# Performance work log

Measured on AMD Instinct MI355X. Metric: run time of the kernel, lower is better.

The kernel has to match this reference:

```python
import jax, jax.numpy as jnp
import numpy as np

N, E, IN, HID, H, L, G = 50000, 500000, 64, 128, 4, 3, 64
C = HID // H


def setup_inputs() -> dict:
    key = jax.random.key(0)
    ks = jax.random.split(key, 24)
    def lin(k, i, o):
        return jax.random.normal(k, (i, o), jnp.float32) * (1.0 / np.sqrt(i))
    d = {}
    d["x"] = jax.random.normal(ks[0], (N, IN), jnp.float32)
    d["edge_index"] = jax.random.randint(ks[1], (2, E), 0, N, jnp.int32)
    d["batch"] = jnp.sort(jax.random.randint(ks[2], (N,), 0, G, jnp.int32))
    # layer 0 (in_dim -> hidden)
    d["l0_Wq"] = lin(ks[3], IN, HID); d["l0_bq"] = jnp.zeros((HID,), jnp.float32)
    d["l0_Wk"] = lin(ks[4], IN, HID); d["l0_bk"] = jnp.zeros((HID,), jnp.float32)
    d["l0_Wv"] = lin(ks[5], IN, HID); d["l0_bv"] = jnp.zeros((HID,), jnp.float32)
    d["l0_Ws"] = lin(ks[6], IN, HID); d["l0_bs"] = jnp.zeros((HID,), jnp.float32)
    d["l0_Wbeta"] = lin(ks[7], 3 * HID, 1)
    d["l0_ln_g"] = jnp.ones((HID,), jnp.float32); d["l0_ln_b"] = jnp.zeros((HID,), jnp.float32)
    # layers 1..L-1 (hidden -> hidden), stacked on leading axis
    M = L - 1
    def slin(k, i, o):
        return jax.random.normal(k, (M, i, o), jnp.float32) * (1.0 / np.sqrt(i))
    d["Wq"] = slin(ks[8], HID, HID); d["bq"] = jnp.zeros((M, HID), jnp.float32)
    d["Wk"] = slin(ks[9], HID, HID); d["bk"] = jnp.zeros((M, HID), jnp.float32)
    d["Wv"] = slin(ks[10], HID, HID); d["bv"] = jnp.zeros((M, HID), jnp.float32)
    d["Ws"] = slin(ks[11], HID, HID); d["bs"] = jnp.zeros((M, HID), jnp.float32)
    d["Wbeta"] = slin(ks[12], 3 * HID, 1)
    d["ln_g"] = jnp.ones((M, HID), jnp.float32); d["ln_b"] = jnp.zeros((M, HID), jnp.float32)
    d["mlp_W1"] = lin(ks[13], HID, HID); d["mlp_b1"] = jnp.zeros((HID,), jnp.float32)
    d["mlp_W2"] = lin(ks[14], HID, 1); d["mlp_b2"] = jnp.zeros((1,), jnp.float32)
    return d


def _conv(x, ei, Wq, bq, Wk, bk, Wv, bv, Ws, bs, Wbeta):
    """PyG TransformerConv with beta=True, concat=True (eval mode, no dropout)."""
    src, dst = ei[0], ei[1]
    q = (x @ Wq + bq).reshape(N, H, C)[dst]   # [E,H,C] target queries
    k = (x @ Wk + bk).reshape(N, H, C)[src]   # [E,H,C] source keys
    v = (x @ Wv + bv).reshape(N, H, C)[src]   # [E,H,C] source values
    alpha = (q * k).sum(-1) / np.sqrt(C)      # [E,H]
    amax = jax.lax.stop_gradient(jax.ops.segment_max(alpha, dst, num_segments=N))
    p = jnp.exp(alpha - amax[dst])
    denom = jax.ops.segment_sum(p, dst, num_segments=N)  # [N,H]
    p = p / denom[dst]                                   # segment softmax per dst node
    out = jax.ops.segment_sum(p[:, :, None] * v, dst, num_segments=N).reshape(N, HID)
    x_r = x @ Ws + bs                                    # root/skip transform
    beta = jax.nn.sigmoid(jnp.concatenate([out, x_r, out - x_r], axis=-1) @ Wbeta)  # [N,1]
    return beta * x_r + (1.0 - beta) * out


def _ln(x, g, b):
    mu = x.mean(-1, keepdims=True)
    var = x.var(-1, keepdims=True)
    return (x - mu) / jnp.sqrt(var + 1e-5) * g + b


def reference(x, edge_index, batch, l0_Wq, l0_bq, l0_Wk, l0_bk, l0_Wv, l0_bv, l0_Ws,
              l0_bs, l0_Wbeta, l0_ln_g, l0_ln_b, Wq, bq, Wk, bk, Wv, bv, Ws, bs,
              Wbeta, ln_g, ln_b, mlp_W1, mlp_b1, mlp_W2, mlp_b2):
    h = _conv(x, edge_index, l0_Wq, l0_bq, l0_Wk, l0_bk, l0_Wv, l0_bv, l0_Ws, l0_bs, l0_Wbeta)
    h = jax.nn.gelu(_ln(h, l0_ln_g, l0_ln_b), approximate=False)
    for i in range(L - 1):
        h = _conv(h, edge_index, Wq[i], bq[i], Wk[i], bk[i], Wv[i], bv[i], Ws[i], bs[i], Wbeta[i])
        h = jax.nn.gelu(_ln(h, ln_g[i], ln_b[i]), approximate=False)
    cnt = jax.ops.segment_sum(jnp.ones((N, 1), h.dtype), batch, num_segments=G)
    g = jax.ops.segment_sum(h, batch, num_segments=G) / jnp.maximum(cnt, 1.0)  # mean pool
    hm = jax.nn.gelu(g @ mlp_W1 + mlp_b1, approximate=False)
    return (hm @ mlp_W2 + mlp_b2).reshape(-1)
```

## Files before the change

### kernel.cpp

```cpp
#include <hip/hip_runtime.h>
#include <hip/hip_bf16.h>
#include <hip/hip_fp16.h>

#define NN 50000
#define EE 500000
#define DIN 64
#define HIDD 128
#define NG 64
#define NB1 49

typedef short short8 __attribute__((ext_vector_type(8)));
typedef float f32x4 __attribute__((ext_vector_type(4)));
typedef _Float16 hf2 __attribute__((ext_vector_type(2)));

#define GLL(g, l)                                                              \
  __builtin_amdgcn_global_load_lds(                                            \
      (const __attribute__((address_space(1))) unsigned*)(g),                  \
      (__attribute__((address_space(3))) unsigned*)(l), 16, 0, 0)

__device__ __forceinline__ unsigned short f2bf(float f) {
  unsigned u = __float_as_uint(f);
  u += 0x7fffu + ((u >> 16) & 1u);
  return (unsigned short)(u >> 16);
}
__device__ __forceinline__ float bfl(unsigned short u) {
  return __uint_as_float((unsigned)u << 16);
}
__device__ __forceinline__ unsigned short f2h(float f) {
  __half h = __float2half(f);
  return *(unsigned short*)&h;
}
__device__ __forceinline__ hf2 u2h2(unsigned u) {
  union { unsigned u; hf2 h; } c; c.u = u; return c.h;
}
__device__ __forceinline__ float dot2h(hf2 a, hf2 b) {
#if __has_builtin(__builtin_amdgcn_fdot2)
  return __builtin_amdgcn_fdot2(a, b, 0.f, false);
#else
  return (float)a.x * (float)b.x + (float)a.y * (float)b.y;
#endif
}

struct BiasW { const float* b[4]; };
struct PrepW { const float* w[12]; };

__global__ __launch_bounds__(256) void count_kernel(const int* __restrict__ ei,
                                                    int* __restrict__ cnt, int E) {
  int e = blockIdx.x * 256 + threadIdx.x;
  if (e < E) atomicAdd(&cnt[ei[E + e]], 1);
}

__global__ __launch_bounds__(1024) void scan1_kernel(const int* __restrict__ cnts,
                                                     int* __restrict__ starts,
                                                     int* __restrict__ btot) {
  __shared__ int sh[1024];
  int t = threadIdx.x;
  int idx = blockIdx.x * 1024 + t;
  int v = (idx < NN) ? cnts[idx] : 0;
  sh[t] = v;
  __syncthreads();
  for (int off = 1; off < 1024; off <<= 1) {
    int add = (t >= off) ? sh[t - off] : 0;
    __syncthreads();
    sh[t] += add;
    __syncthreads();
  }
  if (idx < NN) starts[idx] = sh[t] - v;
  if (t == 1023) btot[blockIdx.x] = sh[1023];
}

__global__ __launch_bounds__(64) void scan2_kernel(const int* __restrict__ btot,
                                                   int* __restrict__ boff,
                                                   int* __restrict__ starts) {
  int t = threadIdx.x;
  int orig = (t < NB1) ? btot[t] : 0;
  int v = orig;
  for (int off = 1; off < 64; off <<= 1) {
    int n_ = __shfl_up(v, off);
    if (t >= off) v += n_;
  }
  if (t < NB1) boff[t] = v - orig;
  if (t == NB1 - 1) starts[NN] = v;
}

__global__ __launch_bounds__(256) void scan3_kernel(int* __restrict__ starts,
                                                    const int* __restrict__ boff,
                                                    int* __restrict__ pos) {
  int i = blockIdx.x * 256 + threadIdx.x;
  if (i < NN) {
    int s = starts[i] + boff[i >> 10];
    starts[i] = s;
    pos[i] = s;
  }
}

__global__ __launch_bounds__(256) void scatter_kernel(const int* __restrict__ ei,
                                                      int* __restrict__ pos,
                                                      int* __restrict__ csr_src, int E) {
  int e = blockIdx.x * 256 + threadIdx.x;
  if (e < 8) csr_src[E + e] = 0;
  if (e < E) {
    int dst = ei[E + e];
    int p = atomicAdd(&pos[dst], 1);
    csr_src[p] = ei[e];
  }
}

__global__ __launch_bounds__(256) void prep_kernel(PrepW pw, short* __restrict__ wT) {
  int o = blockIdx.x * 256 + threadIdx.x;
  if (o >= 163840) return;
  int m, local, K;
  if (o < 32768) { m = o >> 13; local = o & 8191; K = 64; }
  else { int oo = o - 32768; m = 4 + (oo >> 14); local = oo & 16383; K = 128; }
  int col = local / K;
  int off = (local % K) * 2;
  int sw = off ^ ((col & 7) << 4);
  int k = (sw >> 4) * 8 + ((sw & 15) >> 1);
  wT[o] = (short)f2bf(pw.w[m][(size_t)k * 128 + col]);
}

template <int K, bool BF16IN>
__global__ __launch_bounds__(256) void gemm_mat(
    const void* __restrict__ hin, const short* __restrict__ wT, BiasW bw,
    unsigned short* __restrict__ qb, unsigned short* __restrict__ kvb,
    unsigned short* __restrict__ sb, int N) {
  constexpr int RB = 2 * K;
  constexpr int CALLS = (128 * RB) / 4096;
  const float QSC = 0.17677669529663687f;
  __shared__ short bS[128 * K];
  const int mat = blockIdx.y;
  const short* __restrict__ wm = wT + (size_t)mat * 128 * K;
  const int t = threadIdx.x, l = t & 63, wv = t >> 6;

  {
    const char* g0 = (const char*)wm;
    char* lp = (char*)bS;
#pragma unroll
    for (int i = 0; i < CALLS; ++i)
      GLL(g0 + i * 4096 + wv * 1024 + l * 16, lp + i * 4096 + wv * 1024);
  }
  __syncthreads();

  const int lr = l & 15, lk = l >> 4;
  const float* __restrict__ bias = bw.b[mat];

  for (int r0 = blockIdx.x * 64 + wv * 16; r0 < N; r0 += gridDim.x * 64) {
    const int gr = r0 + lr;
    const bool ok = gr < N;
    short8 hfrag[K / 32];
    if (BF16IN) {
      const short* hs = (const short*)hin;
#pragma unroll
      for (int ks = 0; ks < K / 32; ++ks) {
        short8 z = {0, 0, 0, 0, 0, 0, 0, 0};
        hfrag[ks] = ok ? *(const short8*)(hs + (size_t)gr * K + ks * 32 + lk * 8) : z;
      }
    } else {
      const float* hf = (const float*)hin;
#pragma unroll
      for (int ks = 0; ks < K / 32; ++ks) {
        short8 pk = {0, 0, 0, 0, 0, 0, 0, 0};
        if (ok) {
          const float* hp = hf + (size_t)gr * K + ks * 32 + lk * 8;
          f32x4 f0 = *(const f32x4*)hp;
          f32x4 f1 = *(const f32x4*)(hp + 4);
          pk[0] = f2bf(f0.x); pk[1] = f2bf(f0.y); pk[2] = f2bf(f0.z); pk[3] = f2bf(f0.w);
          pk[4] = f2bf(f1.x); pk[5] = f2bf(f1.y); pk[6] = f2bf(f1.z); pk[7] = f2bf(f1.w);
        }
        hfrag[ks] = pk;
      }
    }

    f32x4 acc[8] = {};
#pragma unroll
    for (int ks = 0; ks < K / 32; ++ks) {
#pragma unroll
      for (int cf = 0; cf < 8; ++cf) {
        int col = cf * 16 + lr;
        unsigned bb = col * RB + ((((ks * 4 + lk) * 16)) ^ ((col & 7) << 4));
        short8 w8 = *(const short8*)((const char*)bS + bb);
        acc[cf] = __builtin_amdgcn_mfma_f32_16x16x32_bf16(w8, hfrag[ks], acc[cf], 0, 0, 0);
      }
    }

    if (gr < N) {
#pragma unroll
      for (int cf = 0; cf < 8; ++cf) {
        int ch0 = cf * 16 + lk * 4;
        f32x4 b4 = *(const f32x4*)&bias[ch0];
        float v0 = acc[cf][0] + b4.x, v1 = acc[cf][1] + b4.y;
        float v2 = acc[cf][2] + b4.z, v3 = acc[cf][3] + b4.w;
        if (mat == 0) {
          ushort4 o;
          o.x = f2h(v0 * QSC); o.y = f2h(v1 * QSC);
          o.z = f2h(v2 * QSC); o.w = f2h(v3 * QSC);
          *(ushort4*)&qb[(size_t)gr * 128 + ch0] = o;
        } else if (mat == 3) {
          ushort4 o;
          o.x = f2bf(v0); o.y = f2bf(v1); o.z = f2bf(v2); o.w = f2bf(v3);
          *(ushort4*)&sb[(size_t)gr * 128 + ch0] = o;
        } else {
          unsigned u0 = (unsigned)f2h(v0) | ((unsigned)f2h(v1) << 16);
          unsigned u1 = (unsigned)f2h(v2) | ((unsigned)f2h(v3) << 16);
          unsigned* kvr = (unsigned*)kvb + (size_t)gr * 128;
          int base = ch0 + (mat == 2 ? 1 : 0);
          kvr[base] = u0;
          kvr[base + 2] = u1;
        }
      }
    }
  }
}

template <int NB, bool MASK>
__device__ __forceinline__ void att_batch(
    const int* __restrict__ csr, int i, int s1, const unsigned* __restrict__ kvu,
    int lane, hf2 qp, float& d, float& o0, float& o1) {
  int ce = csr[i + (lane & (NB - 1))];
  uint2 w[NB];
#pragma unroll
  for (int e = 0; e < NB; ++e) {
    int s = __builtin_amdgcn_readlane(ce, e);
    w[e] = *((const uint2*)kvu + ((size_t)s << 6) + lane);
  }
#pragma unroll
  for (int e = 0; e < NB; ++e) {
    float part = dot2h(u2h2(w[e].x), qp);
    part += __shfl_xor(part, 1);
    part += __shfl_xor(part, 2);
    part += __shfl_xor(part, 4);
    part += __shfl_xor(part, 8);
    float p = __expf(part);
    if (MASK) p = (i + e < s1) ? p : 0.f;
    d += p;
    __half2 vh = *(__half2*)&w[e].y;
    float2 vf = __half22float2(vh);
    o0 = fmaf(p, vf.x, o0);
    o1 = fmaf(p, vf.y, o1);
  }
}

__global__ __launch_bounds__(256, 8) void attn_fused(
    const unsigned short* __restrict__ qb, const unsigned* __restrict__ kvu,
    const unsigned short* __restrict__ sb, const int* __restrict__ starts,
    const int* __restrict__ csr, const float* __restrict__ Wbeta,
    const float* __restrict__ lng, const float* __restrict__ lnb,
    unsigned short* __restrict__ hout, int N) {
  int wid = (blockIdx.x * 256 + threadIdx.x) >> 6;
  if (wid >= N) return;
  const int lane = threadIdx.x & 63;
  hf2 qp = u2h2(((const unsigned*)qb)[(size_t)wid * 64 + lane]);
  int s0 = starts[wid], s1 = starts[wid + 1];
  float d = 0.f, o0 = 0.f, o1 = 0.f;
  int i = s0;
  for (; i + 8 <= s1; i += 8)
    att_batch<8, false>(csr, i, s1, kvu, lane, qp, d, o0, o1);
  if (i < s1) {
    if (s1 - i <= 4)
      att_batch<4, true>(csr, i, s1, kvu, lane, qp, d, o0, o1);
    else
      att_batch<8, true>(csr, i, s1, kvu, lane, qp, d, o0, o1);
  }
  float inv = d > 0.f ? 1.f / d : 0.f;
  o0 *= inv; o1 *= inv;
  unsigned su = ((const unsigned*)sb)[(size_t)wid * 64 + lane];
  float sx = bfl((unsigned short)su), sy = bfl((unsigned short)(su >> 16));
  float2 wbo = *(const float2*)&Wbeta[2 * lane];
  float2 wbx = *(const float2*)&Wbeta[128 + 2 * lane];
  float2 wbd = *(const float2*)&Wbeta[256 + 2 * lane];
  float bl = o0 * wbo.x + o1 * wbo.y + sx * wbx.x + sy * wbx.y
           + (o0 - sx) * wbd.x + (o1 - sy) * wbd.y;
  bl += __shfl_xor(bl, 1);  bl += __shfl_xor(bl, 2);  bl += __shfl_xor(bl, 4);
  bl += __shfl_xor(bl, 8);  bl += __shfl_xor(bl, 16); bl += __shfl_xor(bl, 32);
  float beta = 1.f / (1.f + __expf(-bl));
  float hx = beta * sx + (1.f - beta) * o0;
  float hy = beta * sy + (1.f - beta) * o1;
  float s = hx + hy, sq = hx * hx + hy * hy;
  s += __shfl_xor(s, 1);  sq += __shfl_xor(sq, 1);
  s += __shfl_xor(s, 2);  sq += __shfl_xor(sq, 2);
  s += __shfl_xor(s, 4);  sq += __shfl_xor(sq, 4);
  s += __shfl_xor(s, 8);  sq += __shfl_xor(sq, 8);
  s += __shfl_xor(s, 16); sq += __shfl_xor(sq, 16);
  s += __shfl_xor(s, 32); sq += __shfl_xor(sq, 32);
  float mu = s * (1.f / 128.f);
  float var = sq * (1.f / 128.f) - mu * mu;
  float rstd = 1.f / sqrtf(var + 1e-5f);
  float2 g2 = *(const float2*)&lng[2 * lane];
  float2 b2 = *(const float2*)&lnb[2 * lane];
  float y0 = (hx - mu) * rstd * g2.x + b2.x;
  float y1 = (hy - mu) * rstd * g2.y + b2.y;
  y0 = 0.5f * y0 * (1.f + erff(y0 * 0.70710678118654752f));
  y1 = 0.5f * y1 * (1.f + erff(y1 * 0.70710678118654752f));
  unsigned outw = (unsigned)f2bf(y0) | ((unsigned)f2bf(y1) << 16);
  ((unsigned*)hout)[(size_t)wid * 64 + lane] = outw;
}

__global__ __launch_bounds__(256) void pool_kernel(const unsigned short* __restrict__ h,
    const int* __restrict__ batch, float* __restrict__ g,
    float* __restrict__ gcnt, int N) {
  __shared__ float accS[NG * HIDD];
  __shared__ float cntS[NG];
  int t = threadIdx.x;
  for (int i = t; i < NG * HIDD; i += 256) accS[i] = 0.f;
  if (t < NG) cntS[t] = 0.f;
  __syncthreads();
  int lane = t & 63, grp = t >> 6;
  const unsigned* h32 = (const unsigned*)h;
  for (int n = blockIdx.x * 4 + grp; n < N; n += gridDim.x * 4) {
    int b = batch[n];
    unsigned u = h32[(size_t)n * 64 + lane];
    atomicAdd(&accS[b * HIDD + (lane << 1)], __uint_as_float(u << 16));
    atomicAdd(&accS[b * HIDD + (lane << 1) + 1], __uint_as_float(u & 0xffff0000u));
    if (lane == 0) atomicAdd(&cntS[b], 1.f);
  }
  __syncthreads();
  for (int i = t; i < NG * HIDD; i += 256)
    if (accS[i] != 0.f) atomicAdd(&g[i], accS[i]);
  if (t < NG && cntS[t] != 0.f) atomicAdd(&gcnt[t], cntS[t]);
}

__global__ __launch_bounds__(128) void final_kernel(const float* __restrict__ g,
    const float* __restrict__ gcnt, const float* __restrict__ W1,
    const float* __restrict__ b1, const float* __restrict__ W2,
    const float* __restrict__ b2, float* __restrict__ out) {
  __shared__ float gS[HIDD];
  __shared__ float red[2];
  const int gr = blockIdx.x, t = threadIdx.x;
  float cnt = fmaxf(gcnt[gr], 1.f);
  gS[t] = g[gr * HIDD + t] / cnt;
  __syncthreads();
  float s = b1[t];
#pragma unroll 4
  for (int k = 0; k < HIDD; ++k) s = fmaf(gS[k], W1[k * HIDD + t], s);
  s = 0.5f * s * (1.f + erff(s * 0.70710678118654752f));
  float p = s * W2[t];
  p += __shfl_xor(p, 1);  p += __shfl_xor(p, 2);  p += __shfl_xor(p, 4);
  p += __shfl_xor(p, 8);  p += __shfl_xor(p, 16); p += __shfl_xor(p, 32);
  if ((t & 63) == 0) red[t >> 6] = p;
  __syncthreads();
  if (t == 0) out[gr] = red[0] + red[1] + b2[0];
}

extern "C" void kernel_launch(void* const* d_in, const int* in_sizes, int n_in,
                              void* d_out, int out_size, void* d_ws, size_t ws_size,
                              hipStream_t stream) {
  const float* x        = (const float*)d_in[0];
  const int*   ei       = (const int*)d_in[1];
  const int*   batch    = (const int*)d_in[2];
  const float* l0_Wq    = (const float*)d_in[3];
  const float* l0_bq    = (const float*)d_in[4];
  const float* l0_Wk    = (const float*)d_in[5];
  const float* l0_bk    = (const float*)d_in[6];
  const float* l0_Wv    = (const float*)d_in[7];
  const float* l0_bv    = (const float*)d_in[8];
  const float* l0_Ws    = (const float*)d_in[9];
  const float* l0_bs    = (const float*)d_in[10];
  const float* l0_Wbeta = (const float*)d_in[11];
  const float* l0_lng   = (const float*)d_in[12];
  const float* l0_lnb   = (const float*)d_in[13];
  const float* Wq       = (const float*)d_in[14];
  const float* bq       = (const float*)d_in[15];
  const float* Wk       = (const float*)d_in[16];
  const float* bk       = (const float*)d_in[17];
  const float* Wv       = (const float*)d_in[18];
  const float* bv       = (const float*)d_in[19];
  const float* Ws       = (const float*)d_in[20];
  const float* bs       = (const float*)d_in[21];
  const float* Wbeta    = (const float*)d_in[22];
  const float* lng      = (const float*)d_in[23];
  const float* lnb      = (const float*)d_in[24];
  const float* mlp_W1   = (const float*)d_in[25];
  const float* mlp_b1   = (const float*)d_in[26];
  const float* mlp_W2   = (const float*)d_in[27];
  const float* mlp_b2   = (const float*)d_in[28];
  float* outp = (float*)d_out;

  char* ws = (char*)d_ws;
  size_t off = 0;
  auto alloc = [&](size_t bytes) -> void* {
    void* p = ws + off;
    off = (off + bytes + 255) & ~(size_t)255;
    return p;
  };
  unsigned short* h0  = (unsigned short*)alloc((size_t)NN * HIDD * 2);
  unsigned short* h1  = (unsigned short*)alloc((size_t)NN * HIDD * 2);
  unsigned short* qbv = (unsigned short*)alloc((size_t)NN * HIDD * 2);
  unsigned short* sbv = (unsigned short*)alloc((size_t)NN * HIDD * 2);
  unsigned short* kvb = (unsigned short*)alloc((size_t)NN * 256 * 2);
  short*  wT     = (short*)alloc((size_t)163840 * 2);
  int*    starts = (int*)alloc((size_t)(NN + 1) * 4);
  int*    pos    = (int*)alloc((size_t)NN * 4);
  int*    csr    = (int*)alloc((size_t)(EE + 8) * 4);
  int*    btot   = (int*)alloc((size_t)NB1 * 4);
  int*    boff   = (int*)alloc((size_t)NB1 * 4);
  float*  g      = (float*)alloc((size_t)NG * HIDD * 4);
  float*  gcnt   = (float*)alloc((size_t)NG * 4);
  (void)ws_size; (void)in_sizes; (void)n_in; (void)out_size;

  PrepW pw = {{l0_Wq, l0_Wk, l0_Wv, l0_Ws,
               Wq, Wk, Wv, Ws,
               Wq + 16384, Wk + 16384, Wv + 16384, Ws + 16384}};
  prep_kernel<<<640, 256, 0, stream>>>(pw, wT);

  hipMemsetAsync(pos, 0, (size_t)NN * 4, stream);
  count_kernel<<<(EE + 255) / 256, 256, 0, stream>>>(ei, pos, EE);
  scan1_kernel<<<NB1, 1024, 0, stream>>>(pos, starts, btot);
  scan2_kernel<<<1, 64, 0, stream>>>(btot, boff, starts);
  scan3_kernel<<<(NN + 255) / 256, 256, 0, stream>>>(starts, boff, pos);
  scatter_kernel<<<(EE + 255) / 256, 256, 0, stream>>>(ei, pos, csr, EE);

  dim3 ggrid(256, 4);
  int agrid = (NN + 3) / 4;
  const unsigned* kvu = (const unsigned*)kvb;

  BiasW b0 = {{l0_bq, l0_bk, l0_bv, l0_bs}};
  gemm_mat<DIN, false><<<ggrid, 256, 0, stream>>>(x, wT, b0, qbv, kvb, sbv, NN);
  attn_fused<<<agrid, 256, 0, stream>>>(qbv, kvu, sbv, starts, csr, l0_Wbeta,
                                        l0_lng, l0_lnb, h0, NN);

  BiasW b1s = {{bq, bk, bv, bs}};
  gemm_mat<HIDD, true><<<ggrid, 256, 0, stream>>>(h0, wT + 32768, b1s, qbv, kvb, sbv, NN);
  attn_fused<<<agrid, 256, 0, stream>>>(qbv, kvu, sbv, starts, csr, Wbeta,
                                        lng, lnb, h1, NN);

  BiasW b2s = {{bq + HIDD, bk + HIDD, bv + HIDD, bs + HIDD}};
  gemm_mat<HIDD, true><<<ggrid, 256, 0, stream>>>(h1, wT + 98304, b2s, qbv, kvb, sbv, NN);
  attn_fused<<<agrid, 256, 0, stream>>>(qbv, kvu, sbv, starts, csr, Wbeta + 384,
                                        lng + HIDD, lnb + HIDD, h0, NN);

  hipMemsetAsync(g, 0, (size_t)NG * HIDD * 4, stream);
  hipMemsetAsync(gcnt, 0, (size_t)NG * 4, stream);
  pool_kernel<<<256, 256, 0, stream>>>(h0, batch, g, gcnt, NN);
  final_kernel<<<NG, 128, 0, stream>>>(g, gcnt, mlp_W1, mlp_b1, mlp_W2, mlp_b2, outp);
}
```

Baseline: 363.5 us.

## Pair weight matrices per GEMM block and fuse pooling with MLP head

Each GEMM block now computes two projections (q with skip, k with v) from the same loaded input fragments, halving input reads and writing k/v interleaved with a single 16-byte store. Pooling and the final MLP are fused into one kernel per graph that binary-searches the sorted batch array for its node range. This removes the global atomics, two memsets and one launch. In exchange, LDS per GEMM block doubles, which may lower occupancy, and pooling now runs on only 64 blocks.

```diff
diff --git a/kernel.cpp b/kernel.cpp
--- a/kernel.cpp
+++ b/kernel.cpp
@@ -120,29 +120,36 @@
 }
 
 template <int K, bool BF16IN>
-__global__ __launch_bounds__(256) void gemm_mat(
+__global__ __launch_bounds__(256) void gemm_pair(
     const void* __restrict__ hin, const short* __restrict__ wT, BiasW bw,
     unsigned short* __restrict__ qb, unsigned short* __restrict__ kvb,
     unsigned short* __restrict__ sb, int N) {
   constexpr int RB = 2 * K;
   constexpr int CALLS = (128 * RB) / 4096;
   const float QSC = 0.17677669529663687f;
-  __shared__ short bS[128 * K];
-  const int mat = blockIdx.y;
-  const short* __restrict__ wm = wT + (size_t)mat * 128 * K;
+  __shared__ short bS[2][128 * K];
+  const int grp = blockIdx.y;
+  const int m0 = grp ? 1 : 0;
+  const int m1 = grp ? 2 : 3;
   const int t = threadIdx.x, l = t & 63, wv = t >> 6;
 
   {
-    const char* g0 = (const char*)wm;
-    char* lp = (char*)bS;
+    const char* g0 = (const char*)(wT + (size_t)m0 * 128 * K);
+    const char* g1 = (const char*)(wT + (size_t)m1 * 128 * K);
+    char* lp0 = (char*)&bS[0][0];
+    char* lp1 = (char*)&bS[1][0];
 #pragma unroll
     for (int i = 0; i < CALLS; ++i)
-      GLL(g0 + i * 4096 + wv * 1024 + l * 16, lp + i * 4096 + wv * 1024);
+      GLL(g0 + i * 4096 + wv * 1024 + l * 16, lp0 + i * 4096 + wv * 1024);
+#pragma unroll
+    for (int i = 0; i < CALLS; ++i)
+      GLL(g1 + i * 4096 + wv * 1024 + l * 16, lp1 + i * 4096 + wv * 1024);
   }
   __syncthreads();
 
   const int lr = l & 15, lk = l >> 4;
-  const float* __restrict__ bias = bw.b[mat];
+  const float* __restrict__ bias0 = bw.b[m0];
+  const float* __restrict__ bias1 = bw.b[m1];
 
   for (int r0 = blockIdx.x * 64 + wv * 16; r0 < N; r0 += gridDim.x * 64) {
     const int gr = r0 + lr;
@@ -171,15 +178,17 @@
       }
     }
 
-    f32x4 acc[8] = {};
+    f32x4 accA[8] = {}, accB[8] = {};
 #pragma unroll
     for (int ks = 0; ks < K / 32; ++ks) {
 #pragma unroll
       for (int cf = 0; cf < 8; ++cf) {
         int col = cf * 16 + lr;
         unsigned bb = col * RB + ((((ks * 4 + lk) * 16)) ^ ((col & 7) << 4));
-        short8 w8 = *(const short8*)((const char*)bS + bb);
-        acc[cf] = __builtin_amdgcn_mfma_f32_16x16x32_bf16(w8, hfrag[ks], acc[cf], 0, 0, 0);
+        short8 w0 = *(const short8*)((const char*)&bS[0][0] + bb);
+        short8 w1 = *(const short8*)((const char*)&bS[1][0] + bb);
+        accA[cf] = __builtin_amdgcn_mfma_f32_16x16x32_bf16(w0, hfrag[ks], accA[cf], 0, 0, 0);
+        accB[cf] = __builtin_amdgcn_mfma_f32_16x16x32_bf16(w1, hfrag[ks], accB[cf], 0, 0, 0);
       }
     }
 
@@ -187,25 +196,27 @@
 #pragma unroll
       for (int cf = 0; cf < 8; ++cf) {
         int ch0 = cf * 16 + lk * 4;
-        f32x4 b4 = *(const f32x4*)&bias[ch0];
-        float v0 = acc[cf][0] + b4.x, v1 = acc[cf][1] + b4.y;
-        float v2 = acc[cf][2] + b4.z, v3 = acc[cf][3] + b4.w;
-        if (mat == 0) {
-          ushort4 o;
-          o.x = f2h(v0 * QSC); o.y = f2h(v1 * QSC);
-          o.z = f2h(v2 * QSC); o.w = f2h(v3 * QSC);
-          *(ushort4*)&qb[(size_t)gr * 128 + ch0] = o;
-        } else if (mat == 3) {
-          ushort4 o;
-          o.x = f2bf(v0); o.y = f2bf(v1); o.z = f2bf(v2); o.w = f2bf(v3);
-          *(ushort4*)&sb[(size_t)gr * 128 + ch0] = o;
+        f32x4 bA = *(const f32x4*)&bias0[ch0];
+        f32x4 bB = *(const f32x4*)&bias1[ch0];
+        float a0 = accA[cf][0] + bA.x, a1 = accA[cf][1] + bA.y;
+        float a2 = accA[cf][2] + bA.z, a3 = accA[cf][3] + bA.w;
+        float c0 = accB[cf][0] + bB.x, c1 = accB[cf][1] + bB.y;
+        float c2 = accB[cf][2] + bB.z, c3 = accB[cf][3] + bB.w;
+        if (grp == 0) {
+          ushort4 q;
+          q.x = f2h(a0 * QSC); q.y = f2h(a1 * QSC);
+          q.z = f2h(a2 * QSC); q.w = f2h(a3 * QSC);
+          *(ushort4*)&qb[(size_t)gr * 128 + ch0] = q;
+          ushort4 s;
+          s.x = f2bf(c0); s.y = f2bf(c1); s.z = f2bf(c2); s.w = f2bf(c3);
+          *(ushort4*)&sb[(size_t)gr * 128 + ch0] = s;
         } else {
-          unsigned u0 = (unsigned)f2h(v0) | ((unsigned)f2h(v1) << 16);
-          unsigned u1 = (unsigned)f2h(v2) | ((unsigned)f2h(v3) << 16);
-          unsigned* kvr = (unsigned*)kvb + (size_t)gr * 128;
-          int base = ch0 + (mat == 2 ? 1 : 0);
-          kvr[base] = u0;
-          kvr[base + 2] = u1;
+          uint4 o;
+          o.x = (unsigned)f2h(a0) | ((unsigned)f2h(a1) << 16);
+          o.y = (unsigned)f2h(c0) | ((unsigned)f2h(c1) << 16);
+          o.z = (unsigned)f2h(a2) | ((unsigned)f2h(a3) << 16);
+          o.w = (unsigned)f2h(c2) | ((unsigned)f2h(c3) << 16);
+          *(uint4*)((unsigned*)kvb + (size_t)gr * 128 + ch0) = o;
         }
       }
     }
@@ -295,50 +306,52 @@
   ((unsigned*)hout)[(size_t)wid * 64 + lane] = outw;
 }
 
-__global__ __launch_bounds__(256) void pool_kernel(const unsigned short* __restrict__ h,
-    const int* __restrict__ batch, float* __restrict__ g,
-    float* __restrict__ gcnt, int N) {
-  __shared__ float accS[NG * HIDD];
-  __shared__ float cntS[NG];
-  int t = threadIdx.x;
-  for (int i = t; i < NG * HIDD; i += 256) accS[i] = 0.f;
-  if (t < NG) cntS[t] = 0.f;
-  __syncthreads();
-  int lane = t & 63, grp = t >> 6;
-  const unsigned* h32 = (const unsigned*)h;
-  for (int n = blockIdx.x * 4 + grp; n < N; n += gridDim.x * 4) {
-    int b = batch[n];
-    unsigned u = h32[(size_t)n * 64 + lane];
-    atomicAdd(&accS[b * HIDD + (lane << 1)], __uint_as_float(u << 16));
-    atomicAdd(&accS[b * HIDD + (lane << 1) + 1], __uint_as_float(u & 0xffff0000u));
-    if (lane == 0) atomicAdd(&cntS[b], 1.f);
-  }
-  __syncthreads();
-  for (int i = t; i < NG * HIDD; i += 256)
-    if (accS[i] != 0.f) atomicAdd(&g[i], accS[i]);
-  if (t < NG && cntS[t] != 0.f) atomicAdd(&gcnt[t], cntS[t]);
-}
-
-__global__ __launch_bounds__(128) void final_kernel(const float* __restrict__ g,
-    const float* __restrict__ gcnt, const float* __restrict__ W1,
-    const float* __restrict__ b1, const float* __restrict__ W2,
-    const float* __restrict__ b2, float* __restrict__ out) {
+__global__ __launch_bounds__(256) void pool_mlp_kernel(
+    const unsigned short* __restrict__ h, const int* __restrict__ batch,
+    const float* __restrict__ W1, const float* __restrict__ b1,
+    const float* __restrict__ W2, const float* __restrict__ b2,
+    float* __restrict__ out, int N) {
+  __shared__ float accS[4][HIDD];
   __shared__ float gS[HIDD];
   __shared__ float red[2];
-  const int gr = blockIdx.x, t = threadIdx.x;
-  float cnt = fmaxf(gcnt[gr], 1.f);
-  gS[t] = g[gr * HIDD + t] / cnt;
+  const int g = blockIdx.x, t = threadIdx.x;
+  int lo, hi;
+  {
+    int a = 0, b = N;
+    while (a < b) { int m = (a + b) >> 1; if (batch[m] < g) a = m + 1; else b = m; }
+    lo = a;
+    b = N;
+    while (a < b) { int m = (a + b) >> 1; if (batch[m] < g + 1) a = m + 1; else b = m; }
+    hi = a;
+  }
+  const unsigned* h32 = (const unsigned*)h;
+  const int rg = t >> 6, u = t & 63;
+  float a0 = 0.f, a1 = 0.f;
+  for (int n = lo + rg; n < hi; n += 4) {
+    unsigned w = h32[(size_t)n * 64 + u];
+    a0 += bfl((unsigned short)w);
+    a1 += bfl((unsigned short)(w >> 16));
+  }
+  accS[rg][2 * u] = a0;
+  accS[rg][2 * u + 1] = a1;
   __syncthreads();
-  float s = b1[t];
+  if (t < HIDD) {
+    float cnt = fmaxf((float)(hi - lo), 1.f);
+    gS[t] = (accS[0][t] + accS[1][t] + accS[2][t] + accS[3][t]) / cnt;
+  }
+  __syncthreads();
+  if (t < HIDD) {
+    float s = b1[t];
 #pragma unroll 4
-  for (int k = 0; k < HIDD; ++k) s = fmaf(gS[k], W1[k * HIDD + t], s);
-  s = 0.5f * s * (1.f + erff(s * 0.70710678118654752f));
-  float p = s * W2[t];
-  p += __shfl_xor(p, 1);  p += __shfl_xor(p, 2);  p += __shfl_xor(p, 4);
-  p += __shfl_xor(p, 8);  p += __shfl_xor(p, 16); p += __shfl_xor(p, 32);
-  if ((t & 63) == 0) red[t >> 6] = p;
+    for (int k = 0; k < HIDD; ++k) s = fmaf(gS[k], W1[k * HIDD + t], s);
+    s = 0.5f * s * (1.f + erff(s * 0.70710678118654752f));
+    float p = s * W2[t];
+    p += __shfl_xor(p, 1);  p += __shfl_xor(p, 2);  p += __shfl_xor(p, 4);
+    p += __shfl_xor(p, 8);  p += __shfl_xor(p, 16); p += __shfl_xor(p, 32);
+    if ((t & 63) == 0) red[t >> 6] = p;
+  }
   __syncthreads();
-  if (t == 0) out[gr] = red[0] + red[1] + b2[0];
+  if (t == 0) out[g] = red[0] + red[1] + b2[0];
 }
 
 extern "C" void kernel_launch(void* const* d_in, const int* in_sizes, int n_in,
@@ -393,8 +406,6 @@
   int*    csr    = (int*)alloc((size_t)(EE + 8) * 4);
   int*    btot   = (int*)alloc((size_t)NB1 * 4);
   int*    boff   = (int*)alloc((size_t)NB1 * 4);
-  float*  g      = (float*)alloc((size_t)NG * HIDD * 4);
-  float*  gcnt   = (float*)alloc((size_t)NG * 4);
   (void)ws_size; (void)in_sizes; (void)n_in; (void)out_size;
 
   PrepW pw = {{l0_Wq, l0_Wk, l0_Wv, l0_Ws,
@@ -409,27 +420,25 @@
   scan3_kernel<<<(NN + 255) / 256, 256, 0, stream>>>(starts, boff, pos);
   scatter_kernel<<<(EE + 255) / 256, 256, 0, stream>>>(ei, pos, csr, EE);
 
-  dim3 ggrid(256, 4);
+  dim3 ggrid(256, 2);
   int agrid = (NN + 3) / 4;
   const unsigned* kvu = (const unsigned*)kvb;
 
   BiasW b0 = {{l0_bq, l0_bk, l0_bv, l0_bs}};
-  gemm_mat<DIN, false><<<ggrid, 256, 0, stream>>>(x, wT, b0, qbv, kvb, sbv, NN);
+  gemm_pair<DIN, false><<<ggrid, 256, 0, stream>>>(x, wT, b0, qbv, kvb, sbv, NN);
   attn_fused<<<agrid, 256, 0, stream>>>(qbv, kvu, sbv, starts, csr, l0_Wbeta,
                                         l0_lng, l0_lnb, h0, NN);
 
   BiasW b1s = {{bq, bk, bv, bs}};
-  gemm_mat<HIDD, true><<<ggrid, 256, 0, stream>>>(h0, wT + 32768, b1s, qbv, kvb, sbv, NN);
+  gemm_pair<HIDD, true><<<ggrid, 256, 0, stream>>>(h0, wT + 32768, b1s, qbv, kvb, sbv, NN);
   attn_fused<<<agrid, 256, 0, stream>>>(qbv, kvu, sbv, starts, csr, Wbeta,
                                         lng, lnb, h1, NN);
 
   BiasW b2s = {{bq + HIDD, bk + HIDD, bv + HIDD, bs + HIDD}};
-  gemm_mat<HIDD, true><<<ggrid, 256, 0, stream>>>(h1, wT + 98304, b2s, qbv, kvb, sbv, NN);
+  gemm_pair<HIDD, true><<<ggrid, 256, 0, stream>>>(h1, wT + 98304, b2s, qbv, kvb, sbv, NN);
   attn_fused<<<agrid, 256, 0, stream>>>(qbv, kvu, sbv, starts, csr, Wbeta + 384,
                                         lng + HIDD, lnb + HIDD, h0, NN);
 
-  hipMemsetAsync(g, 0, (size_t)NG * HIDD * 4, stream);
-  hipMemsetAsync(gcnt, 0, (size_t)NG * 4, stream);
-  pool_kernel<<<256, 256, 0, stream>>>(h0, batch, g, gcnt, NN);
-  final_kernel<<<NG, 128, 0, stream>>>(g, gcnt, mlp_W1, mlp_b1, mlp_W2, mlp_b2, outp);
-}
+  pool_mlp_kernel<<<NG, 256, 0, stream>>>(h0, batch, mlp_W1, mlp_b1, mlp_W2,
+                                          mlp_b2, outp, NN);
+}
```

After: 350.7 us. 1.04x faster.
